# Kernel tuning notes

Measured on AMD Instinct MI355X. Metric: run time of the kernel, lower is better.

Reference implementation:

```python
import jax, jax.numpy as jnp
import numpy as np

DIM = 576
HEADS = 8
AGENT = 49
GRID_SIZE = 5
ORDER = 3
BN_EPS = 1e-5


def _kan_grid():
    h = 2.0 / GRID_SIZE  # grid_range [-1, 1]
    return jnp.arange(-ORDER, GRID_SIZE + ORDER + 1, dtype=jnp.float32) * h - 1.0


def _bsplines(x, grid):
    # x: (M, in) -> (M, in, GRID_SIZE + ORDER) Cox-de Boor B-spline bases (efficient-kan)
    xe = x[..., None]
    b = ((xe >= grid[:-1]) & (xe < grid[1:])).astype(x.dtype)
    for k in range(1, ORDER + 1):
        b = ((xe - grid[:-(k + 1)]) / (grid[k:-1] - grid[:-(k + 1)]) * b[..., :-1]
             + (grid[k + 1:] - xe) / (grid[k + 1:] - grid[1:-k]) * b[..., 1:])
    return b


def setup_inputs() -> dict:
    key = jax.random.key(0)
    ks = jax.random.split(key, 16)
    b, H, W = 32, 28, 28
    n, c = H * W, DIM
    nrm = lambda k, shape, std=0.02: jax.random.normal(k, shape, jnp.float32) * std
    return {
        "x": jax.random.normal(ks[0], (b, n, c), jnp.float32),
        "H": H,
        "W": W,
        "Wq": nrm(ks[1], (c, c)),
        "Wkv": nrm(ks[2], (2 * c, c)),
        "an_bias": nrm(ks[3], (HEADS, AGENT, 7, 7)),
        "na_bias": nrm(ks[4], (HEADS, AGENT, 7, 7)),
        "ah_bias": nrm(ks[5], (1, HEADS, AGENT, H, 1)),
        "aw_bias": nrm(ks[6], (1, HEADS, AGENT, 1, W)),
        "ha_bias": nrm(ks[7], (1, HEADS, H, 1, AGENT)),
        "wa_bias": nrm(ks[8], (1, HEADS, 1, W, AGENT)),
        "dwc_w": nrm(ks[9], (c, 1, 3, 3), 0.1),
        "dwc_b": jnp.zeros((c,), jnp.float32),
        "bn_gamma": jnp.ones((c,), jnp.float32),
        "bn_beta": jnp.zeros((c,), jnp.float32),
        "bn_mean": jnp.zeros((c,), jnp.float32),
        "bn_var": jnp.ones((c,), jnp.float32),
        "base_weight": nrm(ks[10], (c, c)),
        "spline_weight": nrm(ks[11], (c, c, GRID_SIZE + ORDER)),
        "spline_scaler": jnp.ones((c, c), jnp.float32),
    }


def reference(x, H, W, Wq, Wkv, an_bias, na_bias, ah_bias, aw_bias, ha_bias, wa_bias,
              dwc_w, dwc_b, bn_gamma, bn_beta, bn_mean, bn_var,
              base_weight, spline_weight, spline_scaler):
    b, n, c = x.shape
    h, hd = HEADS, c // HEADS
    scale = hd ** -0.5
    q = x @ Wq.T                       # (b,n,c)
    kv = x @ Wkv.T                     # (b,n,2c)  (sr_ratio == 1)
    k, v = kv[..., :c], kv[..., c:]
    # agent tokens: AdaptiveAvgPool2d(28x28 -> 7x7) == exact 4x4 mean pooling
    p = int(AGENT ** 0.5)
    agent = q.reshape(b, p, H // p, p, W // p, c).mean(axis=(2, 4)).reshape(b, AGENT, c)
    qh = q.reshape(b, n, h, hd).transpose(0, 2, 1, 3)       # (b,h,n,hd)
    kh = k.reshape(b, n, h, hd).transpose(0, 2, 1, 3)
    vh = v.reshape(b, n, h, hd).transpose(0, 2, 1, 3)
    ah = agent.reshape(b, AGENT, h, hd).transpose(0, 2, 1, 3)  # (b,h,A,hd)
    # stage 1: agent tokens attend to k/v (bilinear-upsampled 7x7 bias + separable bias)
    pb1 = jax.image.resize(an_bias, (h, AGENT, H, W), "bilinear").reshape(1, h, AGENT, n)
    pb2 = (ah_bias + aw_bias).reshape(1, h, AGENT, n)
    agent_attn = jax.nn.softmax(jnp.einsum("bhad,bhnd->bhan", ah * scale, kh) + pb1 + pb2, axis=-1)
    agent_v = jnp.einsum("bhan,bhnd->bhad", agent_attn, vh)    # (b,h,A,hd)
    # stage 2: queries attend to agent tokens
    ab1 = jax.image.resize(na_bias, (h, AGENT, H, W), "bilinear").reshape(1, h, AGENT, n).transpose(0, 1, 3, 2)
    ab2 = (ha_bias + wa_bias).reshape(1, h, n, AGENT)
    q_attn = jax.nn.softmax(jnp.einsum("bhnd,bhad->bhna", qh * scale, ah) + ab1 + ab2, axis=-1)
    out = jnp.einsum("bhna,bhad->bhnd", q_attn, agent_v).transpose(0, 2, 1, 3).reshape(b, n, c)
    # depthwise-conv + BN(eval) + ReLU residual on v
    vimg = v.transpose(0, 2, 1).reshape(b, c, H, W)
    y = jax.lax.conv_general_dilated(vimg, dwc_w, (1, 1), "SAME",
                                     feature_group_count=c,
                                     dimension_numbers=("NCHW", "OIHW", "NCHW"))
    y = y + dwc_b[None, :, None, None]
    scale_bn = (bn_gamma / jnp.sqrt(bn_var + BN_EPS))[None, :, None, None]
    y = (y - bn_mean[None, :, None, None]) * scale_bn + bn_beta[None, :, None, None]
    y = jax.nn.relu(y).reshape(b, c, n).transpose(0, 2, 1)
    out = out + y
    # KANLinear projection: silu base branch + B-spline branch
    xf = out.reshape(b * n, c)
    bases = _bsplines(xf, _kan_grid())                           # (M, in, 8)
    scaled = spline_weight * spline_scaler[..., None]            # (out, in, 8)
    proj = jax.nn.silu(xf) @ base_weight.T + jnp.einsum("mik,oik->mo", bases, scaled)
    return proj.reshape(b, n, c)
```

## Files before the change

kernel.cpp:

```cpp
#include <hip/hip_runtime.h>
#include <hip/hip_bf16.h>
#include <math.h>

#define B_ 32
#define N_ 784
#define C_ 576
#define H_ 28
#define W_ 28
#define HEADS_ 8
#define HD_ 72
#define AGENT_ 49
#define M_ (B_ * N_)
#define KTOT_ 5184
#define QKVW_ 1728
#define SCALE_ 0.11785113019775793f

#define SWZ64(row, chunk) (((row) << 6) + ((((chunk) ^ ((row) & 7))) << 3))

typedef unsigned short ushort_t;
typedef __attribute__((ext_vector_type(8))) unsigned short u16x8;
typedef __attribute__((ext_vector_type(8))) __bf16 bf16x8;
typedef __attribute__((ext_vector_type(4))) float f32x4;
typedef __attribute__((ext_vector_type(4))) unsigned u32x4;

__device__ __forceinline__ ushort_t f2bf(float f) {
  union { float f; unsigned u; } v; v.f = f;
  unsigned r = v.u + 0x7fffu + ((v.u >> 16) & 1u);
  return (ushort_t)(r >> 16);
}
__device__ __forceinline__ float bf2f(ushort_t u) {
  union { unsigned u; float f; } v; v.u = ((unsigned)u) << 16;
  return v.f;
}
__device__ __forceinline__ unsigned pack2(float lo, float hi) {
  __bf16 a = (__bf16)lo, b = (__bf16)hi;
  unsigned short ua = __builtin_bit_cast(unsigned short, a);
  unsigned short ub = __builtin_bit_cast(unsigned short, b);
  return (unsigned)ua | ((unsigned)ub << 16);
}
__device__ __forceinline__ void gload16(const ushort_t* g, ushort_t* l) {
  __builtin_amdgcn_global_load_lds(
      (const __attribute__((address_space(1))) unsigned*)g,
      (__attribute__((address_space(3))) unsigned*)l, 16, 0, 0);
}

__device__ __forceinline__ u16x8 packf8(f32x4 a, f32x4 b) {
  u16x8 o;
  o[0]=f2bf(a[0]); o[1]=f2bf(a[1]); o[2]=f2bf(a[2]); o[3]=f2bf(a[3]);
  o[4]=f2bf(b[0]); o[5]=f2bf(b[1]); o[6]=f2bf(b[2]); o[7]=f2bf(b[3]);
  return o;
}

__global__ __launch_bounds__(256) void convert_x_kernel(
    const float* __restrict__ x, ushort_t* __restrict__ xbt) {
  const int totalg = 196 * 9 * 1024;
  for (int g = blockIdx.x * 256 + threadIdx.x; g < totalg; g += gridDim.x * 256) {
    int tile = g >> 10, gi = g & 1023;
    int r = gi >> 3, chp = gi & 7;
    int ch = chp ^ (r & 7);
    int row = (tile / 9) * 128 + r;
    int k0 = (tile % 9) * 64 + ch * 8;
    const float* xp = x + (size_t)row * C_ + k0;
    f32x4 a = *(const f32x4*)xp;
    f32x4 b = *(const f32x4*)(xp + 4);
    *(u16x8*)(xbt + (size_t)tile * 8192 + gi * 8) = packf8(a, b);
  }
}

__global__ __launch_bounds__(256) void pack_w_kernel(
    const float* __restrict__ Wq, const float* __restrict__ Wkv,
    ushort_t* __restrict__ wbt) {
  int tile = blockIdx.x;
  int nt = tile / 9, kw = tile % 9;
  for (int gi = threadIdx.x; gi < 1536; gi += 256) {
    int r = gi >> 3, chp = gi & 7;
    int ch = chp ^ (r & 7);
    int j = nt * 192 + r;
    int k0 = kw * 64 + ch * 8;
    const float* wp = (j < C_) ? (Wq + (size_t)j * C_ + k0)
                               : (Wkv + (size_t)(j - C_) * C_ + k0);
    f32x4 a = *(const f32x4*)wp;
    f32x4 b = *(const f32x4*)(wp + 4);
    *(u16x8*)(wbt + (size_t)tile * 12288 + gi * 8) = packf8(a, b);
  }
}

__global__ __launch_bounds__(256) void pack_b_kernel(
    const float* __restrict__ base_w, const float* __restrict__ spline_w,
    const float* __restrict__ spline_s, ushort_t* __restrict__ btk) {
  int tile = blockIdx.x;
  int nt = tile / 81, kw = tile % 81;
  for (int gi = threadIdx.x; gi < 1536; gi += 256) {
    int r = gi >> 3, chp = gi & 7;
    int ch = chp ^ (r & 7);
    int o = nt * 192 + r;
    int k0 = kw * 64 + ch * 8;
    f32x4 a, b;
    if (k0 < C_) {
      const float* bp = base_w + (size_t)o * C_ + k0;
      a = *(const f32x4*)bp;
      b = *(const f32x4*)(bp + 4);
    } else {
      int i = (k0 - C_) >> 3;
      float sc = spline_s[(size_t)o * C_ + i];
      const float* sp = spline_w + ((size_t)o * C_ + i) * 8;
      a = *(const f32x4*)sp;
      b = *(const f32x4*)(sp + 4);
      a[0]*=sc; a[1]*=sc; a[2]*=sc; a[3]*=sc;
      b[0]*=sc; b[1]*=sc; b[2]*=sc; b[3]*=sc;
    }
    *(u16x8*)(btk + (size_t)tile * 12288 + gi * 8) = packf8(a, b);
  }
}

__device__ __forceinline__ float bilerp7(const float* __restrict__ Bsrc, int y, int x) {
  float sy = y * 0.25f - 0.375f;
  float sx = x * 0.25f - 0.375f;
  float fy0 = floorf(sy), fx0 = floorf(sx);
  int y0 = (int)fy0, x0 = (int)fx0;
  float fy = sy - fy0, fx = sx - fx0;
  int y0c = min(6, max(0, y0)), y1c = min(6, max(0, y0 + 1));
  int x0c = min(6, max(0, x0)), x1c = min(6, max(0, x0 + 1));
  float v00 = Bsrc[y0c * 7 + x0c], v01 = Bsrc[y0c * 7 + x1c];
  float v10 = Bsrc[y1c * 7 + x0c], v11 = Bsrc[y1c * 7 + x1c];
  return (1.f - fy) * ((1.f - fx) * v00 + fx * v01)
       + fy * ((1.f - fx) * v10 + fx * v11);
}

__global__ __launch_bounds__(256) void bias_kernel(
    const float* __restrict__ an_bias, const float* __restrict__ na_bias,
    const float* __restrict__ ah_bias, const float* __restrict__ aw_bias,
    const float* __restrict__ ha_bias, const float* __restrict__ wa_bias,
    float* __restrict__ abias, float* __restrict__ qbias) {
  int idx = blockIdx.x * 256 + threadIdx.x;
  if (idx >= HEADS_ * AGENT_ * N_) return;
  int n = idx % N_;
  int ha = idx / N_;
  int h = ha / AGENT_, a = ha % AGENT_;
  int y = n / W_, x = n % W_;
  float pb1 = bilerp7(an_bias + (size_t)ha * 49, y, x);
  float pb2 = ah_bias[ha * H_ + y] + aw_bias[ha * W_ + x];
  abias[(size_t)ha * N_ + n] = pb1 + pb2;
  float ab1 = bilerp7(na_bias + (size_t)ha * 49, y, x);
  float ab2 = ha_bias[(h * H_ + y) * AGENT_ + a] + wa_bias[(h * W_ + x) * AGENT_ + a];
  qbias[((size_t)h * N_ + n) * AGENT_ + a] = ab1 + ab2;
}

__global__ __launch_bounds__(512, 4) void mfma_qkv_kernel(
    const ushort_t* __restrict__ At, const ushort_t* __restrict__ Bt,
    ushort_t* __restrict__ out) {
  __shared__ ushort_t Asl[2][128 * 64];
  __shared__ ushort_t Bsl[2][192 * 64];
  const int tid = threadIdx.x;
  const int lane = tid & 63, wid = tid >> 6;
  const int wm = wid >> 2, wn = wid & 3;
  const int l16 = lane & 15, lq = lane >> 4;

  int lin = blockIdx.x;
  const int q = 220, r = 4;
  int xcd = lin & 7;
  int wg = (xcd < r ? xcd * (q + 1) : r * (q + 1) + (xcd - r) * q) + (lin >> 3);
  const int m0 = (wg / 9) * 128, n0 = (wg % 9) * 192;

  const ushort_t* aimg = At + (size_t)(wg / 9) * 9 * 8192;
  const ushort_t* bimg = Bt + (size_t)(wg % 9) * 9 * 12288;
  const int aslot = wid * 2;
  const int bslot = wid * 3;

  #pragma unroll
  for (int u = 0; u < 2; ++u)
    gload16(aimg + (size_t)(aslot + u) * 512 + lane * 8, &Asl[0][(aslot + u) * 512]);
  #pragma unroll
  for (int u = 0; u < 3; ++u)
    gload16(bimg + (size_t)(bslot + u) * 512 + lane * 8, &Bsl[0][(bslot + u) * 512]);
  __syncthreads();

  f32x4 acc[4][3] = {};
  const int NSTEP = C_ / 64;
  for (int s = 0; s < NSTEP; ++s) {
    const int cur = s & 1;
    if (s + 1 < NSTEP) {
      const int nxt = cur ^ 1;
      const ushort_t* ai = aimg + (size_t)(s + 1) * 8192;
      const ushort_t* bi = bimg + (size_t)(s + 1) * 12288;
      #pragma unroll
      for (int u = 0; u < 2; ++u)
        gload16(ai + (size_t)(aslot + u) * 512 + lane * 8, &Asl[nxt][(aslot + u) * 512]);
      #pragma unroll
      for (int u = 0; u < 3; ++u)
        gload16(bi + (size_t)(bslot + u) * 512 + lane * 8, &Bsl[nxt][(bslot + u) * 512]);
    }
    #pragma unroll
    for (int ks = 0; ks < 2; ++ks) {
      bf16x8 af[4], bfr[3];
      #pragma unroll
      for (int fm = 0; fm < 4; ++fm)
        af[fm] = *(const bf16x8*)&Asl[cur][SWZ64(wm * 64 + fm * 16 + l16, ks * 4 + lq)];
      #pragma unroll
      for (int fn = 0; fn < 3; ++fn)
        bfr[fn] = *(const bf16x8*)&Bsl[cur][SWZ64(wn * 48 + fn * 16 + l16, ks * 4 + lq)];
      #pragma unroll
      for (int fm = 0; fm < 4; ++fm)
        #pragma unroll
        for (int fn = 0; fn < 3; ++fn)
          acc[fm][fn] = __builtin_amdgcn_mfma_f32_16x16x32_bf16(
              af[fm], bfr[fn], acc[fm][fn], 0, 0, 0);
    }
    __syncthreads();
  }
  #pragma unroll
  for (int fm = 0; fm < 4; ++fm) {
    #pragma unroll
    for (int fn = 0; fn < 3; ++fn) {
      int col = n0 + wn * 48 + fn * 16 + l16;
      #pragma unroll
      for (int r2 = 0; r2 < 4; ++r2) {
        int row = m0 + wm * 64 + fm * 16 + lq * 4 + r2;
        out[(size_t)row * QKVW_ + col] = f2bf(acc[fm][fn][r2]);
      }
    }
  }
}

__device__ __forceinline__ u32x4 basesPack(float xv) {
  float s = __fmaf_rn(xv, 2.5f, 5.5f);
  float tf = floorf(s);
  int t = (int)tf;
  float u = s - tf;
  float u2 = u * u, u3 = u2 * u, um = 1.f - u;
  float p0 = u3 * (1.f / 6.f);
  float p1 = __fmaf_rn(u3, -0.5f, __fmaf_rn(u2, 0.5f, __fmaf_rn(u, 0.5f, 1.f / 6.f)));
  float p2 = __fmaf_rn(u3, 0.5f, __fmaf_rn(u2, -1.f, 2.f / 3.f));
  float p3 = um * um * um * (1.f / 6.f);
  unsigned lo = pack2(p3, p2);
  unsigned hi = pack2(p1, p0);
  unsigned long long packed = ((unsigned long long)hi << 32) | (unsigned long long)lo;
  int sh = t - 3;
  int ba = sh << 4;
  unsigned long long shl_lo = packed << (ba & 63);
  unsigned long long shr_sp = packed >> ((64 - ba) & 63);
  unsigned long long shl_hi = packed << ((ba - 64) & 63);
  unsigned long long shr_ng = packed >> ((-ba) & 63);
  unsigned long long Olo = (sh < 0) ? shr_ng : ((sh < 4) ? shl_lo : 0ull);
  unsigned long long Ohi = (sh <= 0) ? 0ull : ((sh < 4) ? shr_sp : shl_hi);
  if (t < 0 || t > 10) { Olo = 0ull; Ohi = 0ull; }
  u32x4 o;
  o[0] = (unsigned)Olo; o[1] = (unsigned)(Olo >> 32);
  o[2] = (unsigned)Ohi; o[3] = (unsigned)(Ohi >> 32);
  return o;
}

__device__ __forceinline__ u32x4 siluPack(const float* xv) {
  u32x4 o;
  #pragma unroll
  for (int e = 0; e < 4; ++e) {
    float v0 = xv[2 * e], v1 = xv[2 * e + 1];
    float s0 = v0 / (1.f + __expf(-v0));
    float s1 = v1 / (1.f + __expf(-v1));
    o[e] = pack2(s0, s1);
  }
  return o;
}

__global__ __launch_bounds__(512, 4) void kan_mfma_kernel(
    const float* __restrict__ xf, const ushort_t* __restrict__ Bt,
    float* __restrict__ out) {
  __shared__ ushort_t Asl[2][128 * 64];
  __shared__ ushort_t Bsl[2][192 * 64];
  const int tid = threadIdx.x;
  const int lane = tid & 63, wid = tid >> 6;
  const int wm = wid >> 2, wn = wid & 3;
  const int l16 = lane & 15, lq = lane >> 4;

  int lin = blockIdx.x;
  const int q = 73, r = 4;
  int xcd = lin & 7;
  int wg = (xcd < r ? xcd * (q + 1) : r * (q + 1) + (xcd - r) * q) + (lin >> 3);
  const int m0 = (wg / 3) * 128, n0 = (wg % 3) * 192;

  const int srowi = tid >> 3;
  const int chk = tid & 7;

  const float* xfr0 = xf + (size_t)(m0 + srowi) * C_;
  const float* xfr1 = xfr0 + (size_t)64 * C_;
  const ushort_t* bimg = Bt + (size_t)(wg % 3) * 81 * 12288;
  const int bslot = wid * 3;

  const int aW0 = SWZ64(srowi, chk), aW1 = SWZ64(srowi + 64, chk);

  f32x4 acc[4][3] = {};
  float xv0[8], xv1[8];

  #pragma unroll
  for (int u = 0; u < 3; ++u)
    gload16(bimg + (size_t)(bslot + u) * 512 + lane * 8, &Bsl[0][(bslot + u) * 512]);
  {
    f32x4 a = *(const f32x4*)(xfr0 + chk * 8);
    f32x4 b = *(const f32x4*)(xfr0 + chk * 8 + 4);
    xv0[0]=a[0]; xv0[1]=a[1]; xv0[2]=a[2]; xv0[3]=a[3];
    xv0[4]=b[0]; xv0[5]=b[1]; xv0[6]=b[2]; xv0[7]=b[3];
    f32x4 c = *(const f32x4*)(xfr1 + chk * 8);
    f32x4 d = *(const f32x4*)(xfr1 + chk * 8 + 4);
    xv1[0]=c[0]; xv1[1]=c[1]; xv1[2]=c[2]; xv1[3]=c[3];
    xv1[4]=d[0]; xv1[5]=d[1]; xv1[6]=d[2]; xv1[7]=d[3];
  }
  *(u32x4*)&Asl[0][aW0] = siluPack(xv0);
  *(u32x4*)&Asl[0][aW1] = siluPack(xv1);
  {
    f32x4 a = *(const f32x4*)(xfr0 + 64 + chk * 8);
    f32x4 b = *(const f32x4*)(xfr0 + 64 + chk * 8 + 4);
    xv0[0]=a[0]; xv0[1]=a[1]; xv0[2]=a[2]; xv0[3]=a[3];
    xv0[4]=b[0]; xv0[5]=b[1]; xv0[6]=b[2]; xv0[7]=b[3];
    f32x4 c = *(const f32x4*)(xfr1 + 64 + chk * 8);
    f32x4 d = *(const f32x4*)(xfr1 + 64 + chk * 8 + 4);
    xv1[0]=c[0]; xv1[1]=c[1]; xv1[2]=c[2]; xv1[3]=c[3];
    xv1[4]=d[0]; xv1[5]=d[1]; xv1[6]=d[2]; xv1[7]=d[3];
  }
  __syncthreads();

  const int NSTEP = KTOT_ / 64;
  for (int s = 0; s < NSTEP; ++s) {
    const int cur = s & 1;
    if (s + 1 < NSTEP) {
      const int nxt = cur ^ 1;
      const ushort_t* bi = bimg + (size_t)(s + 1) * 12288;
      #pragma unroll
      for (int u = 0; u < 3; ++u)
        gload16(bi + (size_t)(bslot + u) * 512 + lane * 8, &Bsl[nxt][(bslot + u) * 512]);
      const int kg = (s + 1) * 64;
      u32x4 a0, a1;
      if (kg < C_) { a0 = siluPack(xv0); a1 = siluPack(xv1); }
      else         { a0 = basesPack(xv0[0]); a1 = basesPack(xv1[0]); }
      *(u32x4*)&Asl[nxt][aW0] = a0;
      *(u32x4*)&Asl[nxt][aW1] = a1;
      if (s + 2 < NSTEP) {
        const int kl = (s + 2) * 64;
        if (kl < C_) {
          f32x4 a = *(const f32x4*)(xfr0 + kl + chk * 8);
          f32x4 b = *(const f32x4*)(xfr0 + kl + chk * 8 + 4);
          xv0[0]=a[0]; xv0[1]=a[1]; xv0[2]=a[2]; xv0[3]=a[3];
          xv0[4]=b[0]; xv0[5]=b[1]; xv0[6]=b[2]; xv0[7]=b[3];
          f32x4 c = *(const f32x4*)(xfr1 + kl + chk * 8);
          f32x4 d = *(const f32x4*)(xfr1 + kl + chk * 8 + 4);
          xv1[0]=c[0]; xv1[1]=c[1]; xv1[2]=c[2]; xv1[3]=c[3];
          xv1[4]=d[0]; xv1[5]=d[1]; xv1[6]=d[2]; xv1[7]=d[3];
        } else {
          int i0 = ((kl - C_) >> 3) + chk;
          xv0[0] = xfr0[i0];
          xv1[0] = xfr1[i0];
        }
      }
    }
    #pragma unroll
    for (int ks = 0; ks < 2; ++ks) {
      bf16x8 af[4], bfr[3];
      #pragma unroll
      for (int fm = 0; fm < 4; ++fm)
        af[fm] = *(const bf16x8*)&Asl[cur][SWZ64(wm * 64 + fm * 16 + l16, ks * 4 + lq)];
      #pragma unroll
      for (int fn = 0; fn < 3; ++fn)
        bfr[fn] = *(const bf16x8*)&Bsl[cur][SWZ64(wn * 48 + fn * 16 + l16, ks * 4 + lq)];
      #pragma unroll
      for (int fm = 0; fm < 4; ++fm)
        #pragma unroll
        for (int fn = 0; fn < 3; ++fn)
          acc[fm][fn] = __builtin_amdgcn_mfma_f32_16x16x32_bf16(
              af[fm], bfr[fn], acc[fm][fn], 0, 0, 0);
    }
    __syncthreads();
  }
  #pragma unroll
  for (int fm = 0; fm < 4; ++fm) {
    #pragma unroll
    for (int fn = 0; fn < 3; ++fn) {
      int col = n0 + wn * 48 + fn * 16 + l16;
      #pragma unroll
      for (int r2 = 0; r2 < 4; ++r2) {
        int row = m0 + wm * 64 + fm * 16 + lq * 4 + r2;
        out[(size_t)row * C_ + col] = acc[fm][fn][r2];
      }
    }
  }
}

__global__ __launch_bounds__(576) void agent_pool_kernel(
    const ushort_t* __restrict__ qkvb, float* __restrict__ agent) {
  int ba = blockIdx.x;
  int b = ba / AGENT_, a = ba % AGENT_;
  int ay = a / 7, ax = a % 7;
  int ch = threadIdx.x;
  float s = 0.f;
  #pragma unroll
  for (int i2 = 0; i2 < 4; ++i2)
    #pragma unroll
    for (int i4 = 0; i4 < 4; ++i4)
      s += bf2f(qkvb[((size_t)b * N_ + (ay * 4 + i2) * W_ + (ax * 4 + i4)) * QKVW_ + ch]);
  agent[(size_t)ba * C_ + ch] = s * 0.0625f;
}

#define AKS_ 104
#define VTS_ 136
__global__ __launch_bounds__(256) void agent_attn_mfma_kernel(
    const float* __restrict__ agent, const ushort_t* __restrict__ qkvb,
    const float* __restrict__ abias, float* __restrict__ agent_v) {
  __shared__ ushort_t A_lds[64 * AKS_];
  __shared__ ushort_t K_lds[112 * AKS_];
  __shared__ ushort_t Vt_lds[80 * VTS_];
  __shared__ ushort_t P_lds[4][16 * VTS_];
  const int tid = threadIdx.x;
  const int lane = tid & 63, wid = tid >> 6;
  const int l16 = lane & 15, lq = lane >> 4;
  const int b = blockIdx.x >> 3, h = blockIdx.x & 7;

  for (int i = tid; i < 64 * AKS_; i += 256) A_lds[i] = 0;
  for (int i = tid; i < 112 * 32; i += 256) {
    int r = i >> 5, cc = 72 + (i & 31);
    K_lds[r * AKS_ + cc] = 0;
  }
  for (int i = tid; i < 80 * VTS_; i += 256) Vt_lds[i] = 0;
  for (int i = tid; i < 4 * 16 * 24; i += 256) {
    int w = i / (16 * 24), rest = i % (16 * 24);
    int r = rest / 24, cc = 112 + rest % 24;
    P_lds[w][r * VTS_ + cc] = 0;
  }
  for (int i = tid; i < AGENT_ * HD_; i += 256) {
    int a = i / HD_, d = i % HD_;
    A_lds[a * AKS_ + d] = f2bf(agent[((size_t)b * AGENT_ + a) * C_ + h * HD_ + d]);
  }

  int srow[4], scol[4]; bool sval[4];
  #pragma unroll
  for (int i = 0; i < 4; ++i) {
    int idx = tid + i * 256;
    srow[i] = idx / 9; scol[i] = idx % 9;
    sval[i] = idx < 1008;
  }
  const ushort_t* kbase = qkvb + (size_t)b * N_ * QKVW_ + C_ + h * HD_;
  const ushort_t* vbase = qkvb + (size_t)b * N_ * QKVW_ + 2 * C_ + h * HD_;

  u16x8 kreg[4], vreg[4];
  #pragma unroll
  for (int i = 0; i < 4; ++i) {
    if (sval[i]) {
      kreg[i] = *(const u16x8*)(kbase + (size_t)srow[i] * QKVW_ + scol[i] * 8);
      vreg[i] = *(const u16x8*)(vbase + (size_t)srow[i] * QKVW_ + scol[i] * 8);
    }
  }
  #pragma unroll
  for (int i = 0; i < 4; ++i) {
    if (sval[i]) {
      *(u16x8*)&K_lds[srow[i] * AKS_ + scol[i] * 8] = kreg[i];
      #pragma unroll
      for (int e = 0; e < 8; ++e)
        Vt_lds[(scol[i] * 8 + e) * VTS_ + srow[i]] = vreg[i][e];
    }
  }
  __syncthreads();

  float m_r[4] = {-1e30f, -1e30f, -1e30f, -1e30f};
  float l_r[4] = {};
  f32x4 O[5] = {};
  const float* bias_base[4];
  #pragma unroll
  for (int r = 0; r < 4; ++r) {
    int a = wid * 16 + lq * 4 + r;
    a = min(a, AGENT_ - 1);
    bias_base[r] = abias + ((size_t)h * AGENT_ + a) * N_;
  }

  for (int c = 0; c < 7; ++c) {
    if (c < 6) {
      const size_t off = (size_t)(c + 1) * 112 * QKVW_;
      #pragma unroll
      for (int i = 0; i < 4; ++i) {
        if (sval[i]) {
          kreg[i] = *(const u16x8*)(kbase + off + (size_t)srow[i] * QKVW_ + scol[i] * 8);
          vreg[i] = *(const u16x8*)(vbase + off + (size_t)srow[i] * QKVW_ + scol[i] * 8);
        }
      }
    }
    f32x4 sacc[7] = {};
    #pragma unroll
    for (int ks = 0; ks < 3; ++ks) {
      bf16x8 af = *(const bf16x8*)&A_lds[(wid * 16 + l16) * AKS_ + ks * 32 + lq * 8];
      #pragma unroll
      for (int nt = 0; nt < 7; ++nt) {
        bf16x8 bf = *(const bf16x8*)&K_lds[(nt * 16 + l16) * AKS_ + ks * 32 + lq * 8];
        sacc[nt] = __builtin_amdgcn_mfma_f32_16x16x32_bf16(af, bf, sacc[nt], 0, 0, 0);
      }
    }
    float cmax[4] = {-1e30f, -1e30f, -1e30f, -1e30f};
    const int nb = c * 112 + l16;
    #pragma unroll
    for (int nt = 0; nt < 7; ++nt)
      #pragma unroll
      for (int r = 0; r < 4; ++r) {
        float lg = sacc[nt][r] * SCALE_ + bias_base[r][nb + nt * 16];
        sacc[nt][r] = lg;
        cmax[r] = fmaxf(cmax[r], lg);
      }
    #pragma unroll
    for (int off = 1; off < 16; off <<= 1)
      #pragma unroll
      for (int r = 0; r < 4; ++r)
        cmax[r] = fmaxf(cmax[r], __shfl_xor(cmax[r], off));
    float scl[4], rs[4];
    #pragma unroll
    for (int r = 0; r < 4; ++r) {
      float nm = fmaxf(m_r[r], cmax[r]);
      scl[r] = __expf(m_r[r] - nm);
      m_r[r] = nm;
      rs[r] = 0.f;
    }
    #pragma unroll
    for (int nt = 0; nt < 7; ++nt)
      #pragma unroll
      for (int r = 0; r < 4; ++r) {
        float p = __expf(sacc[nt][r] - m_r[r]);
        rs[r] += p;
        P_lds[wid][(lq * 4 + r) * VTS_ + nt * 16 + l16] = f2bf(p);
      }
    #pragma unroll
    for (int off = 1; off < 16; off <<= 1)
      #pragma unroll
      for (int r = 0; r < 4; ++r)
        rs[r] += __shfl_xor(rs[r], off);
    #pragma unroll
    for (int r = 0; r < 4; ++r) l_r[r] = l_r[r] * scl[r] + rs[r];
    #pragma unroll
    for (int nt = 0; nt < 5; ++nt)
      #pragma unroll
      for (int r = 0; r < 4; ++r) O[nt][r] *= scl[r];
    #pragma unroll
    for (int ks = 0; ks < 4; ++ks) {
      bf16x8 pf = *(const bf16x8*)&P_lds[wid][l16 * VTS_ + ks * 32 + lq * 8];
      #pragma unroll
      for (int nt = 0; nt < 5; ++nt) {
        bf16x8 vf = *(const bf16x8*)&Vt_lds[(nt * 16 + l16) * VTS_ + ks * 32 + lq * 8];
        O[nt] = __builtin_amdgcn_mfma_f32_16x16x32_bf16(pf, vf, O[nt], 0, 0, 0);
      }
    }
    __syncthreads();
    if (c < 6) {
      #pragma unroll
      for (int i = 0; i < 4; ++i) {
        if (sval[i]) {
          *(u16x8*)&K_lds[srow[i] * AKS_ + scol[i] * 8] = kreg[i];
          #pragma unroll
          for (int e = 0; e < 8; ++e)
            Vt_lds[(scol[i] * 8 + e) * VTS_ + srow[i]] = vreg[i][e];
        }
      }
      __syncthreads();
    }
  }
  float inv[4];
  #pragma unroll
  for (int r = 0; r < 4; ++r) inv[r] = 1.f / l_r[r];
  #pragma unroll
  for (int nt = 0; nt < 5; ++nt) {
    int d = nt * 16 + l16;
    if (d >= HD_) continue;
    #pragma unroll
    for (int r = 0; r < 4; ++r) {
      int a = wid * 16 + lq * 4 + r;
      if (a < AGENT_)
        agent_v[(((size_t)b * HEADS_ + h) * AGENT_ + a) * HD_ + d] = O[nt][r] * inv[r];
    }
  }
}

__global__ __launch_bounds__(256) void q_attn_kernel(
    const ushort_t* __restrict__ qkvb, const float* __restrict__ agent,
    const float* __restrict__ agent_v, const float* __restrict__ qbias,
    float* __restrict__ xf) {
  __shared__ float ag_t[HD_ * 52];
  __shared__ float av_t[HD_ * 52];
  const int tid = threadIdx.x;
  const int h = blockIdx.y, b = blockIdx.z;
  for (int t = tid; t < AGENT_ * HD_; t += 256) {
    int a = t / HD_, d = t % HD_;
    ag_t[d * 52 + a] = agent[((size_t)b * AGENT_ + a) * C_ + h * HD_ + d];
    av_t[d * 52 + a] = agent_v[(((size_t)b * HEADS_ + h) * AGENT_ + a) * HD_ + d];
  }
  __syncthreads();
  const int n = blockIdx.x * 256 + tid;
  if (n >= N_) return;
  const ushort_t* qp = qkvb + ((size_t)b * N_ + n) * QKVW_ + h * HD_;
  const float* qb = qbias + ((size_t)h * N_ + n) * AGENT_;
  float lg[AGENT_];
  #pragma unroll
  for (int a = 0; a < AGENT_; ++a) lg[a] = qb[a];
  for (int d = 0; d < HD_; ++d) {
    float qd = bf2f(qp[d]) * SCALE_;
    #pragma unroll
    for (int a = 0; a < AGENT_; ++a) lg[a] += qd * ag_t[d * 52 + a];
  }
  float mx = -1e30f;
  #pragma unroll
  for (int a = 0; a < AGENT_; ++a) mx = fmaxf(mx, lg[a]);
  float s = 0.f;
  #pragma unroll
  for (int a = 0; a < AGENT_; ++a) { lg[a] = __expf(lg[a] - mx); s += lg[a]; }
  float inv = 1.f / s;
  #pragma unroll
  for (int a = 0; a < AGENT_; ++a) lg[a] *= inv;
  float* op = xf + ((size_t)b * N_ + n) * C_ + h * HD_;
  for (int d = 0; d < HD_; ++d) {
    float acc = 0.f;
    #pragma unroll
    for (int a = 0; a < AGENT_; ++a) acc += lg[a] * av_t[d * 52 + a];
    op[d] = acc;
  }
}

__global__ __launch_bounds__(288) void dwc_kernel(
    const ushort_t* __restrict__ qkvb, const float* __restrict__ w,
    const float* __restrict__ bias, const float* __restrict__ gamma,
    const float* __restrict__ beta, const float* __restrict__ mean,
    const float* __restrict__ var, float* __restrict__ xf) {
  int lin = blockIdx.x;
  const int bn = (lin & 7) * 3136 + (lin >> 3);
  const int b = bn / N_, n = bn % N_;
  const int y = n / W_, x = n % W_;
  const int c0 = threadIdx.x * 2;
  float a0 = 0.f, a1 = 0.f;
  #pragma unroll
  for (int ky = 0; ky < 3; ++ky) {
    int yy = y + ky - 1;
    if (yy < 0 || yy >= H_) continue;
    #pragma unroll
    for (int kx = 0; kx < 3; ++kx) {
      int xx = x + kx - 1;
      if (xx < 0 || xx >= W_) continue;
      unsigned v = *(const unsigned*)(qkvb + ((size_t)b * N_ + yy * W_ + xx) * QKVW_ + 2 * C_ + c0);
      a0 += w[c0 * 9 + ky * 3 + kx] * bf2f((ushort_t)(v & 0xffffu));
      a1 += w[(c0 + 1) * 9 + ky * 3 + kx] * bf2f((ushort_t)(v >> 16));
    }
  }
  float s0 = gamma[c0] * rsqrtf(var[c0] + 1e-5f);
  float s1 = gamma[c0 + 1] * rsqrtf(var[c0 + 1] + 1e-5f);
  float r0 = fmaxf((a0 + bias[c0] - mean[c0]) * s0 + beta[c0], 0.f);
  float r1 = fmaxf((a1 + bias[c0 + 1] - mean[c0 + 1]) * s1 + beta[c0 + 1], 0.f);
  float2* xp = (float2*)&xf[(size_t)bn * C_ + c0];
  float2 old = *xp;
  old.x += r0; old.y += r1;
  *xp = old;
}

extern "C" void kernel_launch(void* const* d_in, const int* in_sizes, int n_in,
                              void* d_out, int out_size, void* d_ws, size_t ws_size,
                              hipStream_t stream) {
  const float* x        = (const float*)d_in[0];
  const float* Wq       = (const float*)d_in[3];
  const float* Wkv      = (const float*)d_in[4];
  const float* an_bias  = (const float*)d_in[5];
  const float* na_bias  = (const float*)d_in[6];
  const float* ah_bias  = (const float*)d_in[7];
  const float* aw_bias  = (const float*)d_in[8];
  const float* ha_bias  = (const float*)d_in[9];
  const float* wa_bias  = (const float*)d_in[10];
  const float* dwc_w    = (const float*)d_in[11];
  const float* dwc_b    = (const float*)d_in[12];
  const float* bn_gamma = (const float*)d_in[13];
  const float* bn_beta  = (const float*)d_in[14];
  const float* bn_mean  = (const float*)d_in[15];
  const float* bn_var   = (const float*)d_in[16];
  const float* base_w   = (const float*)d_in[17];
  const float* spline_w = (const float*)d_in[18];
  const float* spline_s = (const float*)d_in[19];

  char* ws = (char*)d_ws;
  ushort_t* qkvb   = (ushort_t*)(ws + 0);
  ushort_t* xbt    = (ushort_t*)(ws + 86704128);
  ushort_t* wbt    = (ushort_t*)(ws + 115605504);
  ushort_t* btk    = (ushort_t*)(ws + 117596160);
  float* agent     = (float*)(ws + 123568128);
  float* agent_v   = (float*)(ws + 127180800);
  float* abias     = (float*)(ws + 130793472);
  float* qbias     = (float*)(ws + 132022784);
  float* xf        = (float*)(ws + 133252096);
  float* out       = (float*)d_out;

  convert_x_kernel<<<dim3(2048), dim3(256), 0, stream>>>(x, xbt);
  pack_w_kernel<<<dim3(81), dim3(256), 0, stream>>>(Wq, Wkv, wbt);
  pack_b_kernel<<<dim3(243), dim3(256), 0, stream>>>(base_w, spline_w, spline_s, btk);
  bias_kernel<<<dim3((HEADS_ * AGENT_ * N_ + 255) / 256), dim3(256), 0, stream>>>(
      an_bias, na_bias, ah_bias, aw_bias, ha_bias, wa_bias, abias, qbias);
  mfma_qkv_kernel<<<dim3(1764), dim3(512), 0, stream>>>(xbt, wbt, qkvb);
  agent_pool_kernel<<<dim3(B_ * AGENT_), dim3(C_), 0, stream>>>(qkvb, agent);
  agent_attn_mfma_kernel<<<dim3(B_ * HEADS_), dim3(256), 0, stream>>>(
      agent, qkvb, abias, agent_v);
  q_attn_kernel<<<dim3(4, HEADS_, B_), dim3(256), 0, stream>>>(
      qkvb, agent, agent_v, qbias, xf);
  dwc_kernel<<<dim3(M_), dim3(288), 0, stream>>>(
      qkvb, dwc_w, dwc_b, bn_gamma, bn_beta, bn_mean, bn_var, xf);
  kan_mfma_kernel<<<dim3(588), dim3(512), 0, stream>>>(xf, btk, out);
}
```

Before: 640.7 us.

## Load KAN B operand directly from global into registers, dropping LDS staging

The KAN GEMM no longer stages the packed weight tile through shared memory. Each wave now reads its B fragments straight from a row-major bf16 weight buffer into registers, with one-step register double-buffering. The pack kernel is rewritten to emit that plain row-major layout. This removes LDS capacity and LDS read traffic for B, but adds uncoalesced strided global loads (each row sits KTOT apart) and duplicates B fetches across the two wm waves.

```diff
diff --git a/kernel.cpp b/kernel.cpp
--- a/kernel.cpp
+++ b/kernel.cpp
@@ -87,29 +87,18 @@
 
 __global__ __launch_bounds__(256) void pack_b_kernel(
     const float* __restrict__ base_w, const float* __restrict__ spline_w,
-    const float* __restrict__ spline_s, ushort_t* __restrict__ btk) {
-  int tile = blockIdx.x;
-  int nt = tile / 81, kw = tile % 81;
-  for (int gi = threadIdx.x; gi < 1536; gi += 256) {
-    int r = gi >> 3, chp = gi & 7;
-    int ch = chp ^ (r & 7);
-    int o = nt * 192 + r;
-    int k0 = kw * 64 + ch * 8;
-    f32x4 a, b;
-    if (k0 < C_) {
-      const float* bp = base_w + (size_t)o * C_ + k0;
-      a = *(const f32x4*)bp;
-      b = *(const f32x4*)(bp + 4);
+    const float* __restrict__ spline_s, ushort_t* __restrict__ bpackb) {
+  int o = blockIdx.x;
+  for (int j = threadIdx.x; j < KTOT_; j += 256) {
+    float v;
+    if (j < C_) {
+      v = base_w[(size_t)o * C_ + j];
     } else {
-      int i = (k0 - C_) >> 3;
-      float sc = spline_s[(size_t)o * C_ + i];
-      const float* sp = spline_w + ((size_t)o * C_ + i) * 8;
-      a = *(const f32x4*)sp;
-      b = *(const f32x4*)(sp + 4);
-      a[0]*=sc; a[1]*=sc; a[2]*=sc; a[3]*=sc;
-      b[0]*=sc; b[1]*=sc; b[2]*=sc; b[3]*=sc;
-    }
-    *(u16x8*)(btk + (size_t)tile * 12288 + gi * 8) = packf8(a, b);
+      int jj = j - C_;
+      int i = jj >> 3, kk = jj & 7;
+      v = spline_w[((size_t)o * C_ + i) * 8 + kk] * spline_s[(size_t)o * C_ + i];
+    }
+    bpackb[(size_t)o * KTOT_ + j] = f2bf(v);
   }
 }
 
@@ -266,7 +255,6 @@
     const float* __restrict__ xf, const ushort_t* __restrict__ Bt,
     float* __restrict__ out) {
   __shared__ ushort_t Asl[2][128 * 64];
-  __shared__ ushort_t Bsl[2][192 * 64];
   const int tid = threadIdx.x;
   const int lane = tid & 63, wid = tid >> 6;
   const int wm = wid >> 2, wn = wid & 3;
@@ -283,17 +271,22 @@
 
   const float* xfr0 = xf + (size_t)(m0 + srowi) * C_;
   const float* xfr1 = xfr0 + (size_t)64 * C_;
-  const ushort_t* bimg = Bt + (size_t)(wg % 3) * 81 * 12288;
-  const int bslot = wid * 3;
+  const ushort_t* bp0 = Bt + (size_t)(n0 + wn * 48 + l16) * KTOT_ + lq * 8;
+  const ushort_t* bp1 = bp0 + (size_t)16 * KTOT_;
+  const ushort_t* bp2 = bp0 + (size_t)32 * KTOT_;
 
   const int aW0 = SWZ64(srowi, chk), aW1 = SWZ64(srowi + 64, chk);
 
   f32x4 acc[4][3] = {};
   float xv0[8], xv1[8];
-
-  #pragma unroll
-  for (int u = 0; u < 3; ++u)
-    gload16(bimg + (size_t)(bslot + u) * 512 + lane * 8, &Bsl[0][(bslot + u) * 512]);
+  u16x8 bcur[2][3], bnxt[2][3];
+
+  #pragma unroll
+  for (int ks = 0; ks < 2; ++ks) {
+    bcur[ks][0] = *(const u16x8*)(bp0 + ks * 32);
+    bcur[ks][1] = *(const u16x8*)(bp1 + ks * 32);
+    bcur[ks][2] = *(const u16x8*)(bp2 + ks * 32);
+  }
   {
     f32x4 a = *(const f32x4*)(xfr0 + chk * 8);
     f32x4 b = *(const f32x4*)(xfr0 + chk * 8 + 4);
@@ -323,13 +316,15 @@
     const int cur = s & 1;
     if (s + 1 < NSTEP) {
       const int nxt = cur ^ 1;
-      const ushort_t* bi = bimg + (size_t)(s + 1) * 12288;
-      #pragma unroll
-      for (int u = 0; u < 3; ++u)
-        gload16(bi + (size_t)(bslot + u) * 512 + lane * 8, &Bsl[nxt][(bslot + u) * 512]);
-      const int kg = (s + 1) * 64;
+      const int kn = (s + 1) * 64;
+      #pragma unroll
+      for (int ks = 0; ks < 2; ++ks) {
+        bnxt[ks][0] = *(const u16x8*)(bp0 + kn + ks * 32);
+        bnxt[ks][1] = *(const u16x8*)(bp1 + kn + ks * 32);
+        bnxt[ks][2] = *(const u16x8*)(bp2 + kn + ks * 32);
+      }
       u32x4 a0, a1;
-      if (kg < C_) { a0 = siluPack(xv0); a1 = siluPack(xv1); }
+      if (kn < C_) { a0 = siluPack(xv0); a1 = siluPack(xv1); }
       else         { a0 = basesPack(xv0[0]); a1 = basesPack(xv1[0]); }
       *(u32x4*)&Asl[nxt][aW0] = a0;
       *(u32x4*)&Asl[nxt][aW1] = a1;
@@ -353,21 +348,25 @@
     }
     #pragma unroll
     for (int ks = 0; ks < 2; ++ks) {
-      bf16x8 af[4], bfr[3];
+      bf16x8 af[4];
       #pragma unroll
       for (int fm = 0; fm < 4; ++fm)
         af[fm] = *(const bf16x8*)&Asl[cur][SWZ64(wm * 64 + fm * 16 + l16, ks * 4 + lq)];
-      #pragma unroll
-      for (int fn = 0; fn < 3; ++fn)
-        bfr[fn] = *(const bf16x8*)&Bsl[cur][SWZ64(wn * 48 + fn * 16 + l16, ks * 4 + lq)];
       #pragma unroll
       for (int fm = 0; fm < 4; ++fm)
         #pragma unroll
         for (int fn = 0; fn < 3; ++fn)
           acc[fm][fn] = __builtin_amdgcn_mfma_f32_16x16x32_bf16(
-              af[fm], bfr[fn], acc[fm][fn], 0, 0, 0);
+              af[fm], __builtin_bit_cast(bf16x8, bcur[ks][fn]), acc[fm][fn], 0, 0, 0);
     }
     __syncthreads();
+    if (s + 1 < NSTEP) {
+      #pragma unroll
+      for (int ks = 0; ks < 2; ++ks)
+        #pragma unroll
+        for (int fn = 0; fn < 3; ++fn)
+          bcur[ks][fn] = bnxt[ks][fn];
+    }
   }
   #pragma unroll
   for (int fm = 0; fm < 4; ++fm) {
@@ -674,7 +673,7 @@
   ushort_t* qkvb   = (ushort_t*)(ws + 0);
   ushort_t* xbt    = (ushort_t*)(ws + 86704128);
   ushort_t* wbt    = (ushort_t*)(ws + 115605504);
-  ushort_t* btk    = (ushort_t*)(ws + 117596160);
+  ushort_t* bpackb = (ushort_t*)(ws + 117596160);
   float* agent     = (float*)(ws + 123568128);
   float* agent_v   = (float*)(ws + 127180800);
   float* abias     = (float*)(ws + 130793472);
@@ -684,7 +683,7 @@
 
   convert_x_kernel<<<dim3(2048), dim3(256), 0, stream>>>(x, xbt);
   pack_w_kernel<<<dim3(81), dim3(256), 0, stream>>>(Wq, Wkv, wbt);
-  pack_b_kernel<<<dim3(243), dim3(256), 0, stream>>>(base_w, spline_w, spline_s, btk);
+  pack_b_kernel<<<dim3(C_), dim3(256), 0, stream>>>(base_w, spline_w, spline_s, bpackb);
   bias_kernel<<<dim3((HEADS_ * AGENT_ * N_ + 255) / 256), dim3(256), 0, stream>>>(
       an_bias, na_bias, ah_bias, aw_bias, ha_bias, wa_bias, abias, qbias);
   mfma_qkv_kernel<<<dim3(1764), dim3(512), 0, stream>>>(xbt, wbt, qkvb);
@@ -695,5 +694,5 @@
       qkvb, agent, agent_v, qbias, xf);
   dwc_kernel<<<dim3(M_), dim3(288), 0, stream>>>(
       qkvb, dwc_w, dwc_b, bn_gamma, bn_beta, bn_mean, bn_var, xf);
-  kan_mfma_kernel<<<dim3(588), dim3(512), 0, stream>>>(xf, btk, out);
-}
+  kan_mfma_kernel<<<dim3(588), dim3(512), 0, stream>>>(xf, bpackb, out);
+}
```

Result: slower. 1.003 ms (+56.6%).
